# Kernel tuning notes

Measured on AMD Instinct MI355X. Metric: run time of the kernel, lower is better.

## Reference

```python
import jax, jax.numpy as jnp
import numpy as np
from jax.scipy.ndimage import map_coordinates

N = 512      # image H=W (x0.shape[2])
A = 30       # number of projection angles (sparse-view CT)
D = 729      # det_count (hardcoded in source)
L = 3        # LayerNo
B = 2        # batch
P = 2048     # FFT padding: next pow2 >= 2*D


def _ramp_filter(size):
    # standard Ram-Lak filter built in spatial domain (skimage/torch-radon style)
    n = np.concatenate((np.arange(1, size // 2 + 1, 2), np.arange(size // 2 - 1, 0, -2)))
    f = np.zeros(size)
    f[0] = 0.25
    f[1::2] = -1.0 / (np.pi * n) ** 2
    return jnp.asarray(2.0 * np.real(np.fft.fft(f))[: size // 2 + 1], dtype=jnp.float32)


def setup_inputs() -> dict:
    key = jax.random.key(0)
    ks = jax.random.split(key, 8)
    x0 = jax.random.normal(ks[0], (B, 1, N, N), jnp.float32)
    sinogram = jax.random.normal(ks[1], (B, 1, A, D), jnp.float32)
    theta = jnp.linspace(0.0, np.pi, A, endpoint=False).astype(jnp.float32)
    theta_label = theta
    # denoiser params, stacked over L unrolled layers
    w1 = jax.random.normal(ks[2], (L, 32, 1, 3, 3), jnp.float32) * 0.1
    b1 = jnp.zeros((L, 32), jnp.float32)
    w2 = jax.random.normal(ks[3], (L, 32, 32, 3, 3), jnp.float32) * 0.05
    b2 = jnp.zeros((L, 32), jnp.float32)
    w3 = jax.random.normal(ks[4], (L, 32, 32, 3, 3), jnp.float32) * 0.05
    b3 = jnp.zeros((L, 32), jnp.float32)
    w4 = jax.random.normal(ks[5], (L, 1, 32, 3, 3), jnp.float32) * 0.05
    steps = jnp.ones((L,), jnp.float32)  # step_n params (requires_grad=False)
    return {"cond": 1, "x0": x0, "sinogram": sinogram, "theta": theta,
            "theta_label": theta_label, "w1": w1, "b1": b1, "w2": w2, "b2": b2,
            "w3": w3, "b3": b3, "w4": w4, "steps": steps}


def _conv(x, w, b=None):
    y = jax.lax.conv_general_dilated(x, w, (1, 1), 'SAME',
                                     dimension_numbers=('NCHW', 'OIHW', 'NCHW'))
    return y if b is None else y + b[None, :, None, None]


def _denoiser(x, w1, b1, w2, b2, w3, b3, w4):
    h = jax.nn.relu(_conv(x, w1, b1))
    h = jax.nn.relu(_conv(h, w2, b2))
    h = jax.nn.relu(_conv(h, w3, b3))
    return _conv(h, w4)


def _geometry(theta):
    # parallel-beam ray sampling grid: rows/cols [A, D, T] with T=D samples (dt=1)
    c = (N - 1) / 2.0
    s = jnp.arange(D, dtype=jnp.float32) - (D - 1) / 2.0  # detector coords
    t = s                                                  # along-ray samples
    cs, sn = jnp.cos(theta), jnp.sin(theta)
    x = s[None, :, None] * cs[:, None, None] - t[None, None, :] * sn[:, None, None]
    y = s[None, :, None] * sn[:, None, None] + t[None, None, :] * cs[:, None, None]
    return y + c, x + c  # rows, cols


def _radon_fwd(imgs, rows, cols):
    # imgs [B,N,N] -> sinogram [B,A,D] via bilinear line-integral sampling
    sample = lambda im: map_coordinates(im, [rows, cols], order=1, mode='constant', cval=0.0)
    return jax.vmap(sample)(imgs).sum(-1)


def _filter_sino(sino, filt):
    F = jnp.fft.rfft(sino, n=P, axis=-1)
    g = jnp.fft.irfft(F * filt, n=P, axis=-1)[..., :D]
    return g * (jnp.pi / (2.0 * A))  # FBP normalization


def _backproj(sino, theta):
    # sino [B,A,D] -> image [B,N,N], linear interp along detector axis
    c = (N - 1) / 2.0
    xs = jnp.arange(N, dtype=jnp.float32) - c
    cs, sn = jnp.cos(theta), jnp.sin(theta)
    sgrid = cs[:, None, None] * xs[None, None, :] + sn[:, None, None] * xs[None, :, None]  # [A,N,N]
    idx = sgrid + (D - 1) / 2.0
    lo = jnp.floor(idx).astype(jnp.int32)
    w = idx - lo
    lo_ok = (lo >= 0) & (lo < D)
    hi_ok = (lo + 1 >= 0) & (lo + 1 < D)
    lo_c = jnp.clip(lo, 0, D - 1)
    hi_c = jnp.clip(lo + 1, 0, D - 1)
    a = jnp.arange(A)[:, None, None]
    v = sino[:, a, lo_c] * jnp.where(lo_ok, 1.0 - w, 0.0) + \
        sino[:, a, hi_c] * jnp.where(hi_ok, w, 0.0)       # [B,A,N,N]
    return v.sum(axis=1)


def reference(cond, x0, sinogram, theta, theta_label, w1, b1, w2, b2, w3, b3, w4, steps):
    rows, cols = _geometry(theta)
    filt = _ramp_filter(P)
    X = x0[:, 0]           # [B,N,N]
    sino = sinogram[:, 0]  # [B,A,D]
    for n in range(L):
        sino_pred = _radon_fwd(X, rows, cols)
        filtered = _filter_sino(sino_pred, filt)
        outputs = _backproj(sino - filtered, theta)
        z = X + steps[n] * outputs
        noise = _denoiser(X[:, None], w1[n], b1[n], w2[n], b2[n], w3[n], b3[n], w4[n])[:, 0]
        filtered_noise = _filter_sino(_radon_fwd(noise, rows, cols), filt)
        outputs_noise = _backproj(filtered_noise, theta)
        X = z + noise - steps[n] * outputs_noise
    Xo = X[:, None]
    return (Xo, Xo, Xo)
```

## Files before the change

kernel.cpp:

```cpp
#include <hip/hip_runtime.h>
#include <hip/hip_bf16.h>

typedef __hip_bfloat16 bf16;
typedef __attribute__((ext_vector_type(8))) short short8;
typedef __attribute__((ext_vector_type(4))) short s4v;
typedef __attribute__((ext_vector_type(4))) float float4v;

#define NN 512
#define NA 30
#define ND 729
#define NB 2
#define NL 3
#define BNN (NB*NN*NN)
#define BAD (NB*NA*ND)

#define PW 520
#define PH 516
#define PIMG (PH*PW)
#define POFF (2*PW + 2)

#define O_CS 0
#define O_SN 32
#define O_XP 64
#define O_YP (O_XP + 2*PIMG)
#define O_SP (O_YP + 2*PIMG)
#define O_Q  (O_SP + BAD)
#define O_WR (O_Q + BAD)
#define O_H  (((O_WR + 34560) + 15) & ~15)

#define H_FLOATS (NB * 32 * NN * NN / 2)

#define WR2_OFF 0
#define WR3_OFF 27648
#define WR4_OFF 55296

__global__ void k_params(const float* __restrict__ theta, float* __restrict__ ws)
{
    int i = threadIdx.x;
    if (i < NA) {
        float t = theta[i];
        ws[O_CS + i] = cosf(t);
        ws[O_SN + i] = sinf(t);
    }
}

__global__ void k_init_pad(const float* __restrict__ x0, float* __restrict__ XP,
                           float* __restrict__ YP)
{
    int idx = blockIdx.x * 256 + threadIdx.x;
    if (idx >= 2 * PIMG) return;
    int b = idx / PIMG, p = idx % PIMG;
    int y = p / PW, x = p % PW;
    bool interior = (y >= 2 && y < 2 + NN && x >= 2 && x < 2 + NN);
    float v = interior ? x0[b * NN * NN + (y - 2) * NN + (x - 2)] : 0.f;
    XP[idx] = v;
    if (!interior) YP[idx] = 0.f;
}

__global__ void k_prep_w(const float* __restrict__ w2, const float* __restrict__ w3,
                         const float* __restrict__ w4, bf16* __restrict__ wr)
{
    int idx = blockIdx.x * 256 + threadIdx.x;
    if (idx < 2 * 27648) {
        const float* w = (idx < 27648) ? w2 : w3;
        int base = (idx < 27648) ? WR2_OFF : WR3_OFF;
        int r = idx % 27648;
        int n = r / 9216; int r2 = r % 9216;
        int tap = r2 / 1024; int r3 = r2 % 1024;
        int co = r3 / 32, ci = r3 % 32;
        wr[base + r] = __float2bfloat16(w[n * 9216 + (co * 32 + ci) * 9 + tap]);
    } else if (idx < 2 * 27648 + 3 * 4608) {
        int r = idx - 2 * 27648;
        int n = r / 4608; int r2 = r % 4608;
        int tap = r2 / 512; int r3 = r2 % 512;
        int co = r3 / 32, ci = r3 % 32;
        float v = (co == 0) ? w4[n * 288 + ci * 9 + tap] : 0.f;
        wr[WR4_OFF + r] = __float2bfloat16(v);
    }
}

__device__ __forceinline__ void isect(float A, float coef, float lo, float hi,
                                      float& tlo, float& thi)
{
    float a = (lo - A) / coef, b = (hi - A) / coef;
    float l = fminf(a, b), h = fmaxf(a, b);
    tlo = fmaxf(tlo, l);
    thi = fminf(thi, h);
}

__global__ __launch_bounds__(256) void k_radon(const float* __restrict__ img,
    const float* __restrict__ ws, float* __restrict__ out)
{
    int b = blockIdx.z, a = blockIdx.y;
    int wave = threadIdx.x >> 6;
    int lane = threadIdx.x & 63;
    int s_off = lane & 7, t_sub = lane >> 3;
    int s = blockIdx.x * 32 + wave * 8 + s_off;
    float cs = ws[O_CS + a], sn = ws[O_SN + a];
    float s_c = (float)s - 364.0f;
    float A_r = 255.5f + s_c * sn;
    float A_c = 255.5f + s_c * cs;

    float tlo = -1e9f, thi = 1e9f;
    isect(A_r, cs, -1.0f, 512.0f, tlo, thi);
    isect(A_c, -sn, -1.0f, 512.0f, tlo, thi);
    float t0f = fmaxf(tlo + 364.0f, 0.0f);
    float t1f = fminf(thi + 364.0f, 728.0f);
    int tb, te;
    if (s >= ND || t0f > t1f) { tb = 729; te = -1; }
    else { tb = (int)ceilf(t0f); te = (int)floorf(t1f); }

    int wb = tb, we = te;
    wb = min(wb, __shfl_xor(wb, 1, 64)); we = max(we, __shfl_xor(we, 1, 64));
    wb = min(wb, __shfl_xor(wb, 2, 64)); we = max(we, __shfl_xor(we, 2, 64));
    wb = min(wb, __shfl_xor(wb, 4, 64)); we = max(we, __shfl_xor(we, 4, 64));

    const float* im = img + b * PIMG;
    float acc = 0.f;
#pragma unroll 2
    for (int t = wb + t_sub; t <= we; t += 8) {
        if (t >= tb && t <= te) {
            float tc = (float)t - 364.0f;
            float r = fmaf(tc, cs, A_r);
            float c = fmaf(-tc, sn, A_c);
            float rf = floorf(r), cf = floorf(c);
            float dr = r - rf, dc = c - cf;
            int idx = (int)rf * PW + (int)cf;
            float v00 = im[idx], v01 = im[idx + 1];
            float v10 = im[idx + PW], v11 = im[idx + PW + 1];
            float top = fmaf(dc, v01 - v00, v00);
            float bot = fmaf(dc, v11 - v10, v10);
            acc = fmaf(dr, bot - top, acc + top);
        }
    }
    acc += __shfl_down(acc, 32, 64);
    acc += __shfl_down(acc, 16, 64);
    acc += __shfl_down(acc, 8, 64);
    if (t_sub == 0 && s < ND) out[(b * NA + a) * ND + s] = acc;
}

__global__ void k_filter(const float* __restrict__ sp, const float* __restrict__ sino,
                         float* __restrict__ q)
{
    __shared__ float row[ND];
    __shared__ float taps[364];
    int ba = blockIdx.y;
    const float* src = sp + ba * ND;
    for (int i = threadIdx.x; i < ND; i += 256) row[i] = src[i];
    const float PI2 = 9.86960440108936f;
    for (int i = threadIdx.x; i < 364; i += 256) {
        float m = (float)(2 * i + 1);
        taps[i] = -2.0f / (PI2 * m * m);
    }
    __syncthreads();
    const float scale = 0.0523598775598299f;
    int d = blockIdx.x * 256 + threadIdx.x;
    if (d < ND) {
        float g0 = 0.5f * row[d], g1 = 0.f;
#pragma unroll 4
        for (int j = 0; j < 364; j += 2) {
            int m0 = 2 * j + 1, m1 = 2 * j + 3;
            float l0 = (d - m0 >= 0) ? row[d - m0] : 0.f;
            float r0 = (d + m0 < ND) ? row[d + m0] : 0.f;
            g0 = fmaf(taps[j], l0 + r0, g0);
            float l1 = (d - m1 >= 0) ? row[d - m1] : 0.f;
            float r1 = (d + m1 < ND) ? row[d + m1] : 0.f;
            g1 = fmaf(taps[j + 1], l1 + r1, g1);
        }
        q[ba * ND + d] = sino[ba * ND + d] - scale * (g0 + g1);
    }
}

__global__ __launch_bounds__(256) void k_backproj_update(const float* __restrict__ q,
    const float* __restrict__ src1, const float* __restrict__ ws,
    const float* __restrict__ steps, int n, float* __restrict__ out,
    float* __restrict__ outcopy)
{
    __shared__ float qt[NA][28];
    __shared__ int dmin_s[NA];
    int b = blockIdx.z;
    int x0 = blockIdx.x * 16, y0 = blockIdx.y * 16;
    int tid = threadIdx.x;
    int lx = tid & 15, ly = tid >> 4;
    const float* qb = q + b * NA * ND;

    for (int idx = tid; idx < NA * 26; idx += 256) {
        int a = idx / 26, j = idx % 26;
        float cs = ws[O_CS + a], sn = ws[O_SN + a];
        float f00 = fmaf(cs, (float)x0 - 255.5f, fmaf(sn, (float)y0 - 255.5f, 364.0f));
        float fmn = f00 + fminf(cs * 15.f, 0.f) + fminf(sn * 15.f, 0.f);
        int dm = (int)floorf(fmn);
        if (j == 0) dmin_s[a] = dm;
        int d = dm + j;
        qt[a][j] = (d >= 0 && d < ND) ? qb[a * ND + d] : 0.f;
    }
    __syncthreads();

    float xc = (float)(x0 + lx) - 255.5f, yc = (float)(y0 + ly) - 255.5f;
    float acc = 0.f;
#pragma unroll
    for (int a = 0; a < NA; a++) {
        float cs = ws[O_CS + a], sn = ws[O_SN + a];
        float f = fmaf(cs, xc, fmaf(sn, yc, 364.0f));
        float lf = floorf(f);
        float w = f - lf;
        int j = (int)lf - dmin_s[a];
        float v0 = qt[a][j], v1 = qt[a][j + 1];
        acc = fmaf(v0, 1.0f - w, fmaf(v1, w, acc));
    }
    int pidx = b * PIMG + (y0 + ly) * PW + (x0 + lx);
    float v = fmaf(steps[n], acc, src1[pidx]);
    out[pidx] = v;
    if (outcopy) {
        int fidx = b * NN * NN + (y0 + ly) * NN + (x0 + lx);
        outcopy[fidx] = v;
        outcopy[fidx + BNN] = v;
        outcopy[fidx + 2 * BNN] = v;
    }
}

__global__ __launch_bounds__(256) void k_conv1_hwc(const float* __restrict__ inb,
    const float* __restrict__ W, const float* __restrict__ B, bf16* __restrict__ outb)
{
    int bz = blockIdx.y;
    const float* in = inb + bz * PIMG;
    bf16* out = outb + (size_t)bz * NN * NN * 32;
    int idx = blockIdx.x * 256 + threadIdx.x;
    int y = idx >> 9, x = idx & (NN - 1);
    float v[9];
#pragma unroll
    for (int dy = 0; dy < 3; dy++)
#pragma unroll
        for (int dx = 0; dx < 3; dx++)
            v[dy * 3 + dx] = in[(y + dy - 1) * PW + (x + dx - 1)];
#pragma unroll
    for (int g = 0; g < 4; g++) {
        short8 pk;
#pragma unroll
        for (int j = 0; j < 8; j++) {
            int co = g * 8 + j;
            float a = B[co];
            const float* w = W + co * 9;
#pragma unroll
            for (int k = 0; k < 9; k++) a = fmaf(v[k], w[k], a);
            a = fmaxf(a, 0.f);
            bf16 h = __float2bfloat16(a);
            pk[j] = *reinterpret_cast<short*>(&h);
        }
        *(short8*)(out + (size_t)idx * 32 + g * 8) = pk;
    }
}

#define SH 8
template<int NCO, bool RELU, bool HASB, bool OUTF32>
__global__ __launch_bounds__(256) void k_conv_stream(const bf16* __restrict__ inb,
    const bf16* __restrict__ Wr, const float* __restrict__ Bs,
    const float* __restrict__ addsrc, void* __restrict__ outv)
{
    int lane = threadIdx.x & 63;
    int wave = threadIdx.x >> 6;
    int n16 = lane & 15, quad = lane >> 4;
    int b = blockIdx.z;
    int x0 = blockIdx.x * 16;
    int y0 = (blockIdx.y * 4 + wave) * SH;
    const bf16* in = inb + (size_t)b * NN * NN * 32;

    short8 wf[9 * NCO];
#pragma unroll
    for (int tap = 0; tap < 9; tap++)
#pragma unroll
        for (int t = 0; t < NCO; t++)
            wf[tap * NCO + t] = *(const short8*)(Wr + ((tap * NCO + t) * 16 + n16) * 32 + quad * 8);

    bool vx[3];
#pragma unroll
    for (int dx = 0; dx < 3; dx++) {
        int xx = x0 + n16 + dx - 1;
        vx[dx] = (xx >= 0) && (xx < NN);
    }

    short8 win[3][3];
    auto loadrow = [&](int yy, short8* dst) {
        if (yy >= 0 && yy < NN) {
            const bf16* rowp = in + (size_t)yy * NN * 32;
#pragma unroll
            for (int dx = 0; dx < 3; dx++) {
                short8 v = {};
                if (vx[dx]) v = *(const short8*)(rowp + (x0 + n16 + dx - 1) * 32 + quad * 8);
                dst[dx] = v;
            }
        } else {
            dst[0] = short8{}; dst[1] = short8{}; dst[2] = short8{};
        }
    };
    loadrow(y0 - 1, win[0]);
    loadrow(y0,     win[1]);

    float4v bias[NCO];
#pragma unroll
    for (int t = 0; t < NCO; t++)
        bias[t] = HASB ? *(const float4v*)(Bs + t * 16 + quad * 4) : (float4v){0.f, 0.f, 0.f, 0.f};

#pragma unroll
    for (int i = 0; i < SH; i++) {
        int y = y0 + i;
        loadrow(y + 1, win[(i + 2) % 3]);
        float4v acc[NCO];
#pragma unroll
        for (int t = 0; t < NCO; t++) acc[t] = bias[t];
#pragma unroll
        for (int dy = 0; dy < 3; dy++) {
            short8* row = win[(i + dy) % 3];
#pragma unroll
            for (int dx = 0; dx < 3; dx++) {
                int tap = dy * 3 + dx;
#pragma unroll
                for (int t = 0; t < NCO; t++)
                    acc[t] = __builtin_amdgcn_mfma_f32_16x16x32_bf16(wf[tap * NCO + t], row[dx], acc[t], 0, 0, 0);
            }
        }
        if (OUTF32) {
            float* out = (float*)outv + b * PIMG;
            if (quad == 0) {
                int pi = y * PW + x0 + n16;
                out[pi] = addsrc[b * PIMG + pi] + acc[0][0];
            }
        } else {
            bf16* out = (bf16*)outv + (size_t)b * NN * NN * 32;
            bf16* pp = out + ((size_t)y * NN + x0 + n16) * 32 + quad * 4;
#pragma unroll
            for (int t = 0; t < NCO; t++) {
                s4v pk;
#pragma unroll
                for (int r = 0; r < 4; r++) {
                    float v = acc[t][r];
                    if (RELU) v = fmaxf(v, 0.f);
                    bf16 h = __float2bfloat16(v);
                    pk[r] = *reinterpret_cast<short*>(&h);
                }
                *(s4v*)(pp + t * 16) = pk;
            }
        }
    }
}

extern "C" void kernel_launch(void* const* d_in, const int* in_sizes, int n_in,
                              void* d_out, int out_size, void* d_ws, size_t ws_size,
                              hipStream_t stream)
{
    const float* x0    = (const float*)d_in[1];
    const float* sg    = (const float*)d_in[2];
    const float* theta = (const float*)d_in[3];
    const float* w1    = (const float*)d_in[5];
    const float* b1    = (const float*)d_in[6];
    const float* w2    = (const float*)d_in[7];
    const float* b2    = (const float*)d_in[8];
    const float* w3    = (const float*)d_in[9];
    const float* b3    = (const float*)d_in[10];
    const float* w4    = (const float*)d_in[11];
    const float* steps = (const float*)d_in[12];

    float* ws = (float*)d_ws;
    float* XP = ws + O_XP + POFF;
    float* YP = ws + O_YP + POFF;
    float* SP = ws + O_SP;
    float* Q  = ws + O_Q;
    bf16* wr  = (bf16*)(ws + O_WR);
    bf16* h1  = (bf16*)(ws + O_H);
    bf16* h2  = (bf16*)(ws + O_H + H_FLOATS);

    k_params<<<1, 32, 0, stream>>>(theta, ws);
    k_init_pad<<<(2 * PIMG + 255) / 256, 256, 0, stream>>>(x0, ws + O_XP, ws + O_YP);
    k_prep_w<<<(2 * 27648 + 3 * 4608 + 255) / 256, 256, 0, stream>>>(w2, w3, w4, wr);

    for (int n = 0; n < NL; n++) {
        k_conv1_hwc<<<dim3(NN * NN / 256, NB), 256, 0, stream>>>(XP, w1 + n * 288, b1 + n * 32, h1);
        k_conv_stream<2, true, true, false><<<dim3(32, 16, NB), 256, 0, stream>>>(
            h1, wr + WR2_OFF + n * 9216, b2 + n * 32, nullptr, h2);
        k_conv_stream<2, true, true, false><<<dim3(32, 16, NB), 256, 0, stream>>>(
            h2, wr + WR3_OFF + n * 9216, b3 + n * 32, nullptr, h1);
        k_conv_stream<1, false, false, true><<<dim3(32, 16, NB), 256, 0, stream>>>(
            h1, wr + WR4_OFF + n * 4608, nullptr, XP, YP);

        k_radon<<<dim3(23, NA, NB), 256, 0, stream>>>(YP, ws, SP);
        k_filter<<<dim3(3, NB * NA), 256, 0, stream>>>(SP, sg, Q);
        k_backproj_update<<<dim3(32, 32, NB), 256, 0, stream>>>(
            Q, YP, ws, steps, n, XP, (n == NL - 1) ? (float*)d_out : nullptr);
    }
}
```

Baseline: 490.0 us.

## Pack radon input into bf16 pair layout and merge setup kernels

Adds a packing kernel that converts the padded image into two bf16-pair copies (even and odd column offsets), so each bilinear sample in the radon projection needs two 32-bit loads instead of four float loads. It also folds the trig-parameter kernel into the weight-prep kernel to save a launch. The trade-offs are an extra pack pass per layer and reduced precision of the projected image, which could shift numerics.

Result: slower. 543.6 us (+10.9%).

```diff
diff --git a/kernel.cpp b/kernel.cpp
--- a/kernel.cpp
+++ b/kernel.cpp
@@ -18,6 +18,8 @@
 #define PH 516
 #define PIMG (PH*PW)
 #define POFF (2*PW + 2)
+#define PWD 260
+#define COPYS (NB*PH*PWD)
 
 #define O_CS 0
 #define O_SN 32
@@ -25,42 +27,26 @@
 #define O_YP (O_XP + 2*PIMG)
 #define O_SP (O_YP + 2*PIMG)
 #define O_Q  (O_SP + BAD)
-#define O_WR (O_Q + BAD)
+#define O_PK (O_Q + BAD)
+#define O_WR (O_PK + 2*COPYS)
 #define O_H  (((O_WR + 34560) + 15) & ~15)
-
 #define H_FLOATS (NB * 32 * NN * NN / 2)
 
 #define WR2_OFF 0
 #define WR3_OFF 27648
 #define WR4_OFF 55296
 
-__global__ void k_params(const float* __restrict__ theta, float* __restrict__ ws)
-{
-    int i = threadIdx.x;
-    if (i < NA) {
-        float t = theta[i];
-        ws[O_CS + i] = cosf(t);
-        ws[O_SN + i] = sinf(t);
-    }
-}
-
-__global__ void k_init_pad(const float* __restrict__ x0, float* __restrict__ XP,
-                           float* __restrict__ YP)
+__global__ void k_prep_all(const float* __restrict__ theta,
+                           const float* __restrict__ w2, const float* __restrict__ w3,
+                           const float* __restrict__ w4, float* __restrict__ ws,
+                           bf16* __restrict__ wr)
 {
     int idx = blockIdx.x * 256 + threadIdx.x;
-    if (idx >= 2 * PIMG) return;
-    int b = idx / PIMG, p = idx % PIMG;
-    int y = p / PW, x = p % PW;
-    bool interior = (y >= 2 && y < 2 + NN && x >= 2 && x < 2 + NN);
-    float v = interior ? x0[b * NN * NN + (y - 2) * NN + (x - 2)] : 0.f;
-    XP[idx] = v;
-    if (!interior) YP[idx] = 0.f;
-}
-
-__global__ void k_prep_w(const float* __restrict__ w2, const float* __restrict__ w3,
-                         const float* __restrict__ w4, bf16* __restrict__ wr)
-{
-    int idx = blockIdx.x * 256 + threadIdx.x;
+    if (idx < NA) {
+        float t = theta[idx];
+        ws[O_CS + idx] = cosf(t);
+        ws[O_SN + idx] = sinf(t);
+    }
     if (idx < 2 * 27648) {
         const float* w = (idx < 27648) ? w2 : w3;
         int base = (idx < 27648) ? WR2_OFF : WR3_OFF;
@@ -79,6 +65,37 @@
     }
 }
 
+__global__ void k_init_pad(const float* __restrict__ x0, float* __restrict__ XP,
+                           float* __restrict__ YP)
+{
+    int idx = blockIdx.x * 256 + threadIdx.x;
+    if (idx >= 2 * PIMG) return;
+    int b = idx / PIMG, p = idx % PIMG;
+    int y = p / PW, x = p % PW;
+    bool interior = (y >= 2 && y < 2 + NN && x >= 2 && x < 2 + NN);
+    float v = interior ? x0[b * NN * NN + (y - 2) * NN + (x - 2)] : 0.f;
+    XP[idx] = v;
+    if (!interior) YP[idx] = 0.f;
+}
+
+__global__ void k_pack(const float* __restrict__ YPb, unsigned int* __restrict__ ypk)
+{
+    int idx = blockIdx.x * 256 + threadIdx.x;
+    if (idx >= COPYS) return;
+    int b = idx / (PH * PWD);
+    int r = idx % (PH * PWD);
+    int y = r / PWD, xd = r % PWD;
+    const float* row = YPb + b * PIMG + y * PW;
+    float a0 = row[2 * xd], a1 = row[2 * xd + 1];
+    float a2 = (xd < PWD - 1) ? row[2 * xd + 2] : 0.f;
+    bf16 h0 = __float2bfloat16(a0), h1 = __float2bfloat16(a1), h2 = __float2bfloat16(a2);
+    unsigned u0 = *reinterpret_cast<unsigned short*>(&h0);
+    unsigned u1 = *reinterpret_cast<unsigned short*>(&h1);
+    unsigned u2 = *reinterpret_cast<unsigned short*>(&h2);
+    ypk[idx] = u0 | (u1 << 16);
+    ypk[idx + COPYS] = u1 | (u2 << 16);
+}
+
 __device__ __forceinline__ void isect(float A, float coef, float lo, float hi,
                                       float& tlo, float& thi)
 {
@@ -88,7 +105,7 @@
     thi = fminf(thi, h);
 }
 
-__global__ __launch_bounds__(256) void k_radon(const float* __restrict__ img,
+__global__ __launch_bounds__(256) void k_radon(const unsigned int* __restrict__ ypk,
     const float* __restrict__ ws, float* __restrict__ out)
 {
     int b = blockIdx.z, a = blockIdx.y;
@@ -115,7 +132,7 @@
     wb = min(wb, __shfl_xor(wb, 2, 64)); we = max(we, __shfl_xor(we, 2, 64));
     wb = min(wb, __shfl_xor(wb, 4, 64)); we = max(we, __shfl_xor(we, 4, 64));
 
-    const float* im = img + b * PIMG;
+    const unsigned int* pkb = ypk + b * PH * PWD;
     float acc = 0.f;
 #pragma unroll 2
     for (int t = wb + t_sub; t <= we; t += 8) {
@@ -125,9 +142,14 @@
             float c = fmaf(-tc, sn, A_c);
             float rf = floorf(r), cf = floorf(c);
             float dr = r - rf, dc = c - cf;
-            int idx = (int)rf * PW + (int)cf;
-            float v00 = im[idx], v01 = im[idx + 1];
-            float v10 = im[idx + PW], v11 = im[idx + PW + 1];
+            int pr = (int)rf + 2, pc = (int)cf + 2;
+            int off = ((pc & 1) ? COPYS : 0) + pr * PWD + (pc >> 1);
+            unsigned w0 = pkb[off];
+            unsigned w1 = pkb[off + PWD];
+            float v00 = __uint_as_float(w0 << 16);
+            float v01 = __uint_as_float(w0 & 0xFFFF0000u);
+            float v10 = __uint_as_float(w1 << 16);
+            float v11 = __uint_as_float(w1 & 0xFFFF0000u);
             float top = fmaf(dc, v01 - v00, v00);
             float bot = fmaf(dc, v11 - v10, v10);
             acc = fmaf(dr, bot - top, acc + top);
@@ -365,13 +387,13 @@
     float* YP = ws + O_YP + POFF;
     float* SP = ws + O_SP;
     float* Q  = ws + O_Q;
+    unsigned int* ypk = (unsigned int*)(ws + O_PK);
     bf16* wr  = (bf16*)(ws + O_WR);
     bf16* h1  = (bf16*)(ws + O_H);
     bf16* h2  = (bf16*)(ws + O_H + H_FLOATS);
 
-    k_params<<<1, 32, 0, stream>>>(theta, ws);
+    k_prep_all<<<(2 * 27648 + 3 * 4608 + 255) / 256, 256, 0, stream>>>(theta, w2, w3, w4, ws, wr);
     k_init_pad<<<(2 * PIMG + 255) / 256, 256, 0, stream>>>(x0, ws + O_XP, ws + O_YP);
-    k_prep_w<<<(2 * 27648 + 3 * 4608 + 255) / 256, 256, 0, stream>>>(w2, w3, w4, wr);
 
     for (int n = 0; n < NL; n++) {
         k_conv1_hwc<<<dim3(NN * NN / 256, NB), 256, 0, stream>>>(XP, w1 + n * 288, b1 + n * 32, h1);
@@ -382,7 +404,8 @@
         k_conv_stream<1, false, false, true><<<dim3(32, 16, NB), 256, 0, stream>>>(
             h1, wr + WR4_OFF + n * 4608, nullptr, XP, YP);
 
-        k_radon<<<dim3(23, NA, NB), 256, 0, stream>>>(YP, ws, SP);
+        k_pack<<<(COPYS + 255) / 256, 256, 0, stream>>>(ws + O_YP, ypk);
+        k_radon<<<dim3(23, NA, NB), 256, 0, stream>>>(ypk, ws, SP);
         k_filter<<<dim3(3, NB * NA), 256, 0, stream>>>(SP, sg, Q);
         k_backproj_update<<<dim3(32, 32, NB), 256, 0, stream>>>(
             Q, YP, ws, steps, n, XP, (n == NL - 1) ? (float*)d_out : nullptr);
```

## Assign one wavefront per detector bin in radon and merge setup kernels

Applied to the files above, without the earlier changes.

The forward projection now gives each wavefront a single detector bin, with all 64 lanes stepping along the ray, instead of splitting a wave across 8 bins with 8 lanes each. This drops the per-wave union of ray ranges and the masked iterations it caused, and uses a full wave reduction at the end. Neighbouring lanes now sample consecutive points along one ray, which changes the memory access pattern, and the grid grows to many more blocks. The theta-parameter and weight-prep kernels are also merged into one launch to save a kernel launch.

New measurement: 483.5 us. Within noise of the previous version (-1.3%).

```diff
diff --git a/kernel.cpp b/kernel.cpp
--- a/kernel.cpp
+++ b/kernel.cpp
@@ -27,40 +27,23 @@
 #define O_Q  (O_SP + BAD)
 #define O_WR (O_Q + BAD)
 #define O_H  (((O_WR + 34560) + 15) & ~15)
-
 #define H_FLOATS (NB * 32 * NN * NN / 2)
 
 #define WR2_OFF 0
 #define WR3_OFF 27648
 #define WR4_OFF 55296
 
-__global__ void k_params(const float* __restrict__ theta, float* __restrict__ ws)
-{
-    int i = threadIdx.x;
-    if (i < NA) {
-        float t = theta[i];
-        ws[O_CS + i] = cosf(t);
-        ws[O_SN + i] = sinf(t);
-    }
-}
-
-__global__ void k_init_pad(const float* __restrict__ x0, float* __restrict__ XP,
-                           float* __restrict__ YP)
+__global__ void k_prep_all(const float* __restrict__ theta,
+                           const float* __restrict__ w2, const float* __restrict__ w3,
+                           const float* __restrict__ w4, float* __restrict__ ws,
+                           bf16* __restrict__ wr)
 {
     int idx = blockIdx.x * 256 + threadIdx.x;
-    if (idx >= 2 * PIMG) return;
-    int b = idx / PIMG, p = idx % PIMG;
-    int y = p / PW, x = p % PW;
-    bool interior = (y >= 2 && y < 2 + NN && x >= 2 && x < 2 + NN);
-    float v = interior ? x0[b * NN * NN + (y - 2) * NN + (x - 2)] : 0.f;
-    XP[idx] = v;
-    if (!interior) YP[idx] = 0.f;
-}
-
-__global__ void k_prep_w(const float* __restrict__ w2, const float* __restrict__ w3,
-                         const float* __restrict__ w4, bf16* __restrict__ wr)
-{
-    int idx = blockIdx.x * 256 + threadIdx.x;
+    if (idx < NA) {
+        float t = theta[idx];
+        ws[O_CS + idx] = cosf(t);
+        ws[O_SN + idx] = sinf(t);
+    }
     if (idx < 2 * 27648) {
         const float* w = (idx < 27648) ? w2 : w3;
         int base = (idx < 27648) ? WR2_OFF : WR3_OFF;
@@ -79,6 +62,19 @@
     }
 }
 
+__global__ void k_init_pad(const float* __restrict__ x0, float* __restrict__ XP,
+                           float* __restrict__ YP)
+{
+    int idx = blockIdx.x * 256 + threadIdx.x;
+    if (idx >= 2 * PIMG) return;
+    int b = idx / PIMG, p = idx % PIMG;
+    int y = p / PW, x = p % PW;
+    bool interior = (y >= 2 && y < 2 + NN && x >= 2 && x < 2 + NN);
+    float v = interior ? x0[b * NN * NN + (y - 2) * NN + (x - 2)] : 0.f;
+    XP[idx] = v;
+    if (!interior) YP[idx] = 0.f;
+}
+
 __device__ __forceinline__ void isect(float A, float coef, float lo, float hi,
                                       float& tlo, float& thi)
 {
@@ -94,8 +90,8 @@
     int b = blockIdx.z, a = blockIdx.y;
     int wave = threadIdx.x >> 6;
     int lane = threadIdx.x & 63;
-    int s_off = lane & 7, t_sub = lane >> 3;
-    int s = blockIdx.x * 32 + wave * 8 + s_off;
+    int s = blockIdx.x * 4 + wave;
+    if (s >= ND) return;
     float cs = ws[O_CS + a], sn = ws[O_SN + a];
     float s_c = (float)s - 364.0f;
     float A_r = 255.5f + s_c * sn;
@@ -106,20 +102,14 @@
     isect(A_c, -sn, -1.0f, 512.0f, tlo, thi);
     float t0f = fmaxf(tlo + 364.0f, 0.0f);
     float t1f = fminf(thi + 364.0f, 728.0f);
-    int tb, te;
-    if (s >= ND || t0f > t1f) { tb = 729; te = -1; }
-    else { tb = (int)ceilf(t0f); te = (int)floorf(t1f); }
-
-    int wb = tb, we = te;
-    wb = min(wb, __shfl_xor(wb, 1, 64)); we = max(we, __shfl_xor(we, 1, 64));
-    wb = min(wb, __shfl_xor(wb, 2, 64)); we = max(we, __shfl_xor(we, 2, 64));
-    wb = min(wb, __shfl_xor(wb, 4, 64)); we = max(we, __shfl_xor(we, 4, 64));
-
-    const float* im = img + b * PIMG;
+
     float acc = 0.f;
+    if (t0f <= t1f) {
+        int tb = (int)ceilf(t0f);
+        int te = (int)floorf(t1f);
+        const float* im = img + b * PIMG;
 #pragma unroll 2
-    for (int t = wb + t_sub; t <= we; t += 8) {
-        if (t >= tb && t <= te) {
+        for (int t = tb + lane; t <= te; t += 64) {
             float tc = (float)t - 364.0f;
             float r = fmaf(tc, cs, A_r);
             float c = fmaf(-tc, sn, A_c);
@@ -136,7 +126,10 @@
     acc += __shfl_down(acc, 32, 64);
     acc += __shfl_down(acc, 16, 64);
     acc += __shfl_down(acc, 8, 64);
-    if (t_sub == 0 && s < ND) out[(b * NA + a) * ND + s] = acc;
+    acc += __shfl_down(acc, 4, 64);
+    acc += __shfl_down(acc, 2, 64);
+    acc += __shfl_down(acc, 1, 64);
+    if (lane == 0) out[(b * NA + a) * ND + s] = acc;
 }
 
 __global__ void k_filter(const float* __restrict__ sp, const float* __restrict__ sino,
@@ -369,9 +362,8 @@
     bf16* h1  = (bf16*)(ws + O_H);
     bf16* h2  = (bf16*)(ws + O_H + H_FLOATS);
 
-    k_params<<<1, 32, 0, stream>>>(theta, ws);
+    k_prep_all<<<(2 * 27648 + 3 * 4608 + 255) / 256, 256, 0, stream>>>(theta, w2, w3, w4, ws, wr);
     k_init_pad<<<(2 * PIMG + 255) / 256, 256, 0, stream>>>(x0, ws + O_XP, ws + O_YP);
-    k_prep_w<<<(2 * 27648 + 3 * 4608 + 255) / 256, 256, 0, stream>>>(w2, w3, w4, wr);
 
     for (int n = 0; n < NL; n++) {
         k_conv1_hwc<<<dim3(NN * NN / 256, NB), 256, 0, stream>>>(XP, w1 + n * 288, b1 + n * 32, h1);
@@ -382,7 +374,7 @@
         k_conv_stream<1, false, false, true><<<dim3(32, 16, NB), 256, 0, stream>>>(
             h1, wr + WR4_OFF + n * 4608, nullptr, XP, YP);
 
-        k_radon<<<dim3(23, NA, NB), 256, 0, stream>>>(YP, ws, SP);
+        k_radon<<<dim3((ND + 3) / 4, NA, NB), 256, 0, stream>>>(YP, ws, SP);
         k_filter<<<dim3(3, NB * NA), 256, 0, stream>>>(SP, sg, Q);
         k_backproj_update<<<dim3(32, 32, NB), 256, 0, stream>>>(
             Q, YP, ws, steps, n, XP, (n == NL - 1) ? (float*)d_out : nullptr);
```
